# Performance work log

Measured on AMD Instinct MI355X. Metric: run time of the kernel, lower is better.

## Reference

```python
import jax, jax.numpy as jnp
import numpy as np

N, E, De, Dv = 40000, 8000, 32, 8   # nodes, hyperedges, edge degree, node degree
D, Q, EIG, VOC, NC = 256, 256, 64, 1000, 40  # vertex/edge dim, query dim, eig dim, centrality vocab, classes
LN_EPS = 1e-5


def _linear(x, W, b):
    return x @ W + b


def _layernorm(x, g, b):
    mu = jnp.mean(x, axis=-1, keepdims=True)
    var = jnp.mean(jnp.square(x - mu), axis=-1, keepdims=True)
    return (x - mu) * jax.lax.rsqrt(var + LN_EPS) * g + b


def setup_inputs() -> dict:
    key = jax.random.key(0)
    ks = iter(jax.random.split(key, 64))
    def nrm(shape, s=0.02):
        return (jax.random.normal(next(ks), shape, jnp.float32) * s).astype(jnp.float32)
    inp = {
        'vfeat': jax.random.normal(next(ks), (N, D), jnp.float32),
        'efeat': jax.random.normal(next(ks), (E, D), jnp.float32),
        'eign_vec': jax.random.normal(next(ks), (N, EIG), jnp.float32),
        'feat_v_gcn': jax.random.normal(next(ks), (N, D), jnp.float32),
        'cent1': jax.random.uniform(next(ks), (E, De), jnp.float32),
        'cent2': jax.random.uniform(next(ks), (N, Dv), jnp.float32),
        'cent_idx': jax.random.randint(next(ks), (N,), 0, VOC),
        'uniq_idx': jax.random.randint(next(ks), (N,), 0, VOC),
        'edge2node': jax.random.randint(next(ks), (E, De), 0, N),
        'node2edge': jax.random.randint(next(ks), (N, Dv), 0, E),
        # learned parameters (W: [in, out])
        'W_vtx': nrm((D, D)), 'b_vtx': jnp.zeros((D,), jnp.float32),
        'W_pe': nrm((EIG, D)), 'b_pe': jnp.zeros((D,), jnp.float32),
        'cs_emb': nrm((VOC, D)), 'un_emb': nrm((VOC, D)),
        'W_kv': nrm((D, Q)), 'b_kv': jnp.zeros((Q,), jnp.float32),
        'W_vv': nrm((D, D)), 'b_vv': jnp.zeros((D,), jnp.float32),
        'W_qe': nrm((D, Q)), 'b_qe': jnp.zeros((Q,), jnp.float32),
        'W_ke': nrm((D, Q)), 'b_ke': jnp.zeros((Q,), jnp.float32),
        'W_ve': nrm((D, D)), 'b_ve': jnp.zeros((D,), jnp.float32),
        'W_qv': nrm((D, Q)), 'b_qv': jnp.zeros((Q,), jnp.float32),
        'W_l1': nrm((D, Q)), 'b_l1': jnp.zeros((Q,), jnp.float32),
        'W_l2': nrm((Q, D)), 'b_l2': jnp.zeros((D,), jnp.float32),
        'W_l3': nrm((D, Q)), 'b_l3': jnp.zeros((Q,), jnp.float32),
        'W_l4': nrm((Q, D)), 'b_l4': jnp.zeros((D,), jnp.float32),
        'ln1_g': jnp.ones((D,), jnp.float32), 'ln1_b': jnp.zeros((D,), jnp.float32),
        'ln2_g': jnp.ones((D,), jnp.float32), 'ln2_b': jnp.zeros((D,), jnp.float32),
        'W_cls': nrm((D, NC)), 'b_cls': jnp.zeros((NC,), jnp.float32),
    }
    return inp


def _forward(vfeat, efeat, eign_vec, feat_v_gcn, cent1, cent2,
             W_vtx, b_vtx, W_pe, b_pe, cs_emb, un_emb,
             W_kv, b_kv, W_vv, b_vv, W_qe, b_qe, W_ke, b_ke, W_ve, b_ve, W_qv, b_qv,
             W_l1, b_l1, W_l2, b_l2, W_l3, b_l3, W_l4, b_l4,
             ln1_g, ln1_b, ln2_g, ln2_b, W_cls, b_cls,
             cent_idx, uniq_idx, edge2node, node2edge):
    scale = 1.0 / np.sqrt(float(W_kv.shape[1]))  # 1/sqrt(query_dim)
    # first_layer feature assembly: vtx_lin_1layer + PE + GCN + centrality/uniqueness embeddings
    feat_v = (_linear(vfeat, W_vtx, b_vtx) + _linear(eign_vec, W_pe, b_pe)
              + feat_v_gcn + cs_emb[cent_idx] + un_emb[uniq_idx])
    feat_e = efeat

    # ---- stage 1: hyperedges attend over member nodes ('in' etype) ----
    k_n = _linear(feat_v, W_kv, b_kv)              # [N,Q]
    v_n = _linear(feat_v, W_vv, b_vv)              # [N,D]
    q_e = _linear(feat_e, W_qe, b_qe)              # [E,Q]
    km = k_n[edge2node]                            # [E,De,Q]
    attn = jax.nn.leaky_relu(jnp.einsum('edq,eq->ed', km, q_e), 0.01) * scale
    score = jax.nn.softmax(attn + cent1, axis=1)   # centrality-biased softmax (k-core + clustering)
    h_e = jnp.einsum('ed,edc->ec', score, v_n[edge2node])  # [E,D]
    x_e = _layernorm(h_e + feat_e, ln1_g, ln1_b)
    f_e = _linear(jax.nn.relu(_linear(x_e, W_l1, b_l1)), W_l2, b_l2)
    feat_e = _layernorm(f_e + x_e, ln1_g, ln1_b)

    # ---- stage 2: nodes attend over incident hyperedges ('con' etype) ----
    k_e = _linear(feat_e, W_ke, b_ke)              # [E,Q]
    v_e = _linear(feat_e, W_ve, b_ve)              # [E,D]
    q_v = _linear(feat_v, W_qv, b_qv)              # [N,Q]
    km2 = k_e[node2edge]                           # [N,Dv,Q]
    attn2 = jax.nn.leaky_relu(jnp.einsum('ndq,nq->nd', km2, q_v), 0.01) * scale
    score2 = jax.nn.softmax(attn2 + cent2, axis=1)
    h_v = jnp.einsum('nd,ndc->nc', score2, v_e[node2edge])  # [N,D]
    x_v = _layernorm(h_v + feat_v, ln2_g, ln2_b)
    f_v = _linear(jax.nn.relu(_linear(x_v, W_l3, b_l3)), W_l4, b_l4)
    feat_v = _layernorm(f_v + x_v, ln2_g, ln2_b)

    # last_layer classification head (dropout is identity in eval)
    return _linear(feat_v, W_cls, b_cls)           # [N,NC]


def reference(vfeat, efeat, eign_vec, feat_v_gcn, cent1, cent2,
              cent_idx, uniq_idx, edge2node, node2edge,
              W_vtx, b_vtx, W_pe, b_pe, cs_emb, un_emb,
              W_kv, b_kv, W_vv, b_vv, W_qe, b_qe, W_ke, b_ke, W_ve, b_ve, W_qv, b_qv,
              W_l1, b_l1, W_l2, b_l2, W_l3, b_l3, W_l4, b_l4,
              ln1_g, ln1_b, ln2_g, ln2_b, W_cls, b_cls):
    return _forward(vfeat, efeat, eign_vec, feat_v_gcn, cent1, cent2,
                    W_vtx, b_vtx, W_pe, b_pe, cs_emb, un_emb,
                    W_kv, b_kv, W_vv, b_vv, W_qe, b_qe, W_ke, b_ke, W_ve, b_ve, W_qv, b_qv,
                    W_l1, b_l1, W_l2, b_l2, W_l3, b_l3, W_l4, b_l4,
                    ln1_g, ln1_b, ln2_g, ln2_b, W_cls, b_cls,
                    cent_idx, uniq_idx, edge2node, node2edge)
```

## Files before the change

kernel.cpp:

```cpp
#include <hip/hip_runtime.h>
#include <hip/hip_bf16.h>
#include <cstddef>

#define N_NODES 40000
#define N_EDGES 8000
#define DE 32
#define DV 8
#define DIM 256
#define QDIM 256
#define EIGD 64
#define NCLS 40
#define LN_EPS 1e-5f
#define ATT_SCALE 0.0625f

typedef unsigned short u16;
typedef unsigned int u32;
using i16x8 = __attribute__((ext_vector_type(8))) short;
using f32x4 = __attribute__((ext_vector_type(4))) float;

__device__ inline u16 f2b(float f) {
    union { float f; u32 u; } c; c.f = f;
    u32 u = c.u + 0x7FFF + ((c.u >> 16) & 1);
    return (u16)(u >> 16);
}
__device__ inline float b2f(u16 b) {
    union { u32 u; float f; } c; c.u = (u32)b << 16;
    return c.f;
}

__device__ inline void gload_lds16(const u16* g, u16* l) {
    __builtin_amdgcn_global_load_lds(
        (const __attribute__((address_space(1))) void*)g,
        (__attribute__((address_space(3))) void*)l, 16, 0, 0);
}

#define VMCNT12 asm volatile("s_waitcnt vmcnt(12)" ::: "memory")
#define VMCNT10 asm volatile("s_waitcnt vmcnt(10)" ::: "memory")
#define VMCNT6  asm volatile("s_waitcnt vmcnt(6)" ::: "memory")
#define VMCNT5  asm volatile("s_waitcnt vmcnt(5)" ::: "memory")
#define VMCNT4  asm volatile("s_waitcnt vmcnt(4)" ::: "memory")
#define VMCNT0  asm volatile("s_waitcnt vmcnt(0)" ::: "memory")
#define LGKM0   asm volatile("s_waitcnt lgkmcnt(0)" ::: "memory")

__global__ __launch_bounds__(256) void prep_weights(
    const float* w0, const float* w1, const float* w2, const float* w3,
    const float* w4, const float* w5, const float* w6, const float* w7,
    const float* w8, const float* w9, const float* w10, const float* w11,
    const float* w12, u16* __restrict__ pool)
{
    const float* srcs[13] = {w0,w1,w2,w3,w4,w5,w6,w7,w8,w9,w10,w11,w12};
    const int Ks[13]  = {256,64,256,256,256,256,256,256,256,256,256,256,256};
    const int Nds[13] = {256,256,256,256,256,256,256,256,256,256,256,256,40};
    const int id = blockIdx.z;
    const float* W = srcs[id];
    u16* Wt = pool + (size_t)id * 65536;
    const int K = Ks[id], Nd = Nds[id];
    const int k0 = blockIdx.x * 32, n0 = blockIdx.y * 32;
    if (k0 >= K || n0 >= Nd) return;

    __shared__ float tile[32][33];
    const int x = threadIdx.x & 31, y4 = (threadIdx.x >> 5) * 4;
#pragma unroll
    for (int j = 0; j < 4; j++) {
        int k = k0 + y4 + j;
        tile[y4 + j][x] = (k < K && (n0 + x) < Nd) ? W[(size_t)k * Nd + n0 + x] : 0.f;
    }
    __syncthreads();
#pragma unroll
    for (int j = 0; j < 4; j++) {
        int n = n0 + y4 + j;
        if (n < Nd && (k0 + x) < K)
            Wt[(size_t)n * K + k0 + x] = f2b(tile[x][y4 + j]);
    }
}

template <int EPI, int AMODE, int NT>
__global__ __launch_bounds__(256, 2) void gemmN(
    const void* __restrict__ Av, const u16* __restrict__ Wt,
    const float* __restrict__ bias0, const float* __restrict__ bias1,
    const float* __restrict__ bias2,
    void* __restrict__ Cv, int Nd)
{
    __shared__ u16 Asm[3][64 * 64];
    __shared__ u16 Bsm[3][128 * 64];
    const int t = threadIdx.x;
    const int lane = t & 63, w = t >> 6;
    const int wr = w >> 1, wc = w & 1;
    const int row0 = blockIdx.y * 64, col0 = blockIdx.x * 128;

    f32x4 acc[2][4] = {};

    const int srow = lane >> 3;
    const int sblk = ((lane & 7) ^ srow) * 8;
    const int fr = lane & 15, h = lane >> 4;
    const int lsw = fr & 7;

    float4 farA[2][2][2];

    auto stage_load = [&](int kt) {
        const int buf = kt % 3;
        const int k0 = kt << 6;
        if constexpr (AMODE == 0) {
#pragma unroll
            for (int i = 0; i < 2; i++) {
                const int r = w * 16 + i * 8;
                gload_lds16((const u16*)Av + (size_t)(row0 + r + srow) * 256 + k0 + sblk,
                            &Asm[buf][r * 64]);
            }
        } else {
#pragma unroll
            for (int i = 0; i < 2; i++) {
                const int r = w * 16 + i * 8;
                const float* ap = (const float*)Av + (size_t)(row0 + r + srow) * 256 + k0 + sblk;
                farA[kt & 1][i][0] = *(const float4*)ap;
                farA[kt & 1][i][1] = *(const float4*)(ap + 4);
            }
        }
#pragma unroll
        for (int i = 0; i < 4; i++) {
            const int r = w * 32 + i * 8;
            int ng = col0 + r + srow; if (ng > Nd - 1) ng = Nd - 1;
            gload_lds16(Wt + (size_t)ng * 256 + k0 + sblk, &Bsm[buf][r * 64]);
        }
    };
    auto stage_write = [&](int kt) {
        const int buf = kt % 3;
#pragma unroll
        for (int i = 0; i < 2; i++) {
            const int r = w * 16 + i * 8;
            float4 f0 = farA[kt & 1][i][0], f1 = farA[kt & 1][i][1];
            i16x8 v;
            v[0] = (short)f2b(f0.x); v[1] = (short)f2b(f0.y);
            v[2] = (short)f2b(f0.z); v[3] = (short)f2b(f0.w);
            v[4] = (short)f2b(f1.x); v[5] = (short)f2b(f1.y);
            v[6] = (short)f2b(f1.z); v[7] = (short)f2b(f1.w);
            *(i16x8*)&Asm[buf][(r + srow) * 64 + (lane & 7) * 8] = v;
        }
    };

    stage_load(0);
    if (NT > 1) stage_load(1);
    if constexpr (AMODE != 0) stage_write(0);

#pragma unroll
    for (int kt = 0; kt < NT; ++kt) {
        const int buf = kt % 3;
        if (kt + 2 < NT) stage_load(kt + 2);
        if constexpr (AMODE != 0) {
            if (kt + 1 < NT) stage_write(kt + 1);
            else { VMCNT0; }
        } else {
            if (kt + 2 < NT) { VMCNT12; }
            else if (kt + 1 < NT) { VMCNT6; }
            else { VMCNT0; }
        }
        __builtin_amdgcn_s_barrier();

        i16x8 af[2][2], bfr[2][4];
#pragma unroll
        for (int kk = 0; kk < 2; kk++) {
#pragma unroll
            for (int m = 0; m < 2; m++)
                af[kk][m] = *(const i16x8*)&Asm[buf][(wr * 32 + m * 16 + fr) * 64 +
                                                    ((kk * 4 + h) ^ lsw) * 8];
#pragma unroll
            for (int n = 0; n < 4; n++)
                bfr[kk][n] = *(const i16x8*)&Bsm[buf][(wc * 64 + n * 16 + fr) * 64 +
                                                     ((kk * 4 + h) ^ lsw) * 8];
        }
        LGKM0;
        __builtin_amdgcn_sched_barrier(0);
        __builtin_amdgcn_s_barrier();

#pragma unroll
        for (int kk = 0; kk < 2; kk++)
#pragma unroll
            for (int m = 0; m < 2; m++)
#pragma unroll
                for (int n = 0; n < 4; n++)
                    acc[m][n] = __builtin_amdgcn_mfma_f32_16x16x32_bf16(
                        af[kk][m], bfr[kk][n], acc[m][n], 0, 0, 0);
    }

    const int seg = (int)(blockIdx.x >> 1);
    const float* bp = (seg == 0) ? bias0 : ((seg == 1) ? bias1 : bias2);
#pragma unroll
    for (int m = 0; m < 2; m++) {
#pragma unroll
        for (int j = 0; j < 4; j++) {
            const int grow = row0 + wr * 32 + m * 16 + h * 4 + j;
#pragma unroll
            for (int n = 0; n < 4; n++) {
                const int gcol = col0 + wc * 64 + n * 16 + fr;
                if (EPI == 4 && gcol >= Nd) continue;
                float v = acc[m][n][j] + bp[gcol & 255];
                if constexpr (EPI == 1) v = fmaxf(v, 0.f);
                if constexpr (EPI == 4)
                    ((float*)Cv)[(size_t)grow * Nd + gcol] = v;
                else
                    ((u16*)Cv)[(size_t)grow * Nd + gcol] = f2b(v);
            }
        }
    }
}

template <int EPI, int AMODE, int NT>
__global__ __launch_bounds__(256, 2) void gemmW(
    const void* __restrict__ Av, const float* __restrict__ A2,
    const u16* __restrict__ Wt, const u16* __restrict__ Wt2,
    const float* __restrict__ bias0, const float* __restrict__ bias1,
    const u16* __restrict__ resid,
    const float* __restrict__ gcn, const float* __restrict__ emb1,
    const float* __restrict__ emb2, const int* __restrict__ idx1,
    const int* __restrict__ idx2, const float* __restrict__ lng,
    const float* __restrict__ lnb, u16* __restrict__ Cv)
{
    __shared__ u16 Asm[3][64 * 32];
    __shared__ u16 Bsm[3][256 * 32];
    const int t = threadIdx.x;
    const int lane = t & 63, w = t >> 6;
    const int row0 = blockIdx.y * 64;

    f32x4 acc[4][4] = {};

    const int srow = lane >> 2;
    const int sblk = ((lane & 3) ^ ((lane >> 3) & 3)) * 8;
    const int fr = lane & 15, h = lane >> 4;
    const int rsw = (fr >> 1) & 3;

    float4 farA[2][2];

    auto stage_load = [&](int kt) {
        const int buf = kt % 3;
        const int k0 = kt << 5;
        const bool tail = (AMODE == 2) && (k0 >= 256);
        if constexpr (AMODE == 0) {
            gload_lds16((const u16*)Av + (size_t)(row0 + w * 16 + srow) * 256 + k0 + sblk,
                        &Asm[buf][(w * 16) * 32]);
        } else {
            const float* ap = tail
                ? A2 + (size_t)(row0 + w * 16 + srow) * 64 + (k0 - 256) + sblk
                : (const float*)Av + (size_t)(row0 + w * 16 + srow) * 256 + k0 + sblk;
            farA[kt & 1][0] = *(const float4*)ap;
            farA[kt & 1][1] = *(const float4*)(ap + 4);
        }
#pragma unroll
        for (int i = 0; i < 4; i++) {
            const int r = w * 64 + i * 16;
            const u16* gp = tail ? Wt2 + (size_t)(r + srow) * 64 + (k0 - 256) + sblk
                                 : Wt + (size_t)(r + srow) * 256 + k0 + sblk;
            gload_lds16(gp, &Bsm[buf][r * 32]);
        }
    };
    auto stage_write = [&](int kt) {
        const int buf = kt % 3;
        float4 f0 = farA[kt & 1][0], f1 = farA[kt & 1][1];
        i16x8 v;
        v[0] = (short)f2b(f0.x); v[1] = (short)f2b(f0.y);
        v[2] = (short)f2b(f0.z); v[3] = (short)f2b(f0.w);
        v[4] = (short)f2b(f1.x); v[5] = (short)f2b(f1.y);
        v[6] = (short)f2b(f1.z); v[7] = (short)f2b(f1.w);
        *(i16x8*)&Asm[buf][(w * 16 + srow) * 32 + (lane & 3) * 8] = v;
    };

    stage_load(0);
    if (NT > 1) stage_load(1);
    if constexpr (AMODE != 0) stage_write(0);

#pragma unroll
    for (int kt = 0; kt < NT; ++kt) {
        const int buf = kt % 3;
        if (kt + 2 < NT) stage_load(kt + 2);
        if constexpr (AMODE != 0) {
            if (kt + 1 < NT) stage_write(kt + 1);
            else { VMCNT0; }
        } else {
            if (kt + 2 < NT) { VMCNT10; }
            else if (kt + 1 < NT) { VMCNT5; }
            else { VMCNT0; }
        }
        __builtin_amdgcn_s_barrier();

        i16x8 af[4], bfr[4];
#pragma unroll
        for (int m = 0; m < 4; m++)
            af[m] = *(const i16x8*)&Asm[buf][(m * 16 + fr) * 32 + (h ^ rsw) * 8];
#pragma unroll
        for (int n = 0; n < 4; n++)
            bfr[n] = *(const i16x8*)&Bsm[buf][(w * 64 + n * 16 + fr) * 32 + (h ^ rsw) * 8];
        LGKM0;
        __builtin_amdgcn_sched_barrier(0);
        __builtin_amdgcn_s_barrier();

#pragma unroll
        for (int m = 0; m < 4; m++)
#pragma unroll
            for (int n = 0; n < 4; n++)
                acc[m][n] = __builtin_amdgcn_mfma_f32_16x16x32_bf16(
                    af[m], bfr[n], acc[m][n], 0, 0, 0);
    }

    if constexpr (EPI == 5) {
        float* redS = (float*)&Asm[0][0];
        float* redQ = redS + 256;
#pragma unroll
        for (int m = 0; m < 4; m++) {
#pragma unroll
            for (int j = 0; j < 4; j++) {
                const int grow = row0 + m * 16 + h * 4 + j;
                float s = 0.f, q = 0.f;
#pragma unroll
                for (int n = 0; n < 4; n++) {
                    const int gcol = w * 64 + n * 16 + fr;
                    float v = acc[m][n][j] + bias0[gcol] +
                              b2f(resid[(size_t)grow * 256 + gcol]);
                    acc[m][n][j] = v;
                    s += v; q += v * v;
                }
#pragma unroll
                for (int off = 1; off < 16; off <<= 1) {
                    s += __shfl_xor(s, off, 64);
                    q += __shfl_xor(q, off, 64);
                }
                if (fr == 0) {
                    redS[(m * 16 + h * 4 + j) * 4 + w] = s;
                    redQ[(m * 16 + h * 4 + j) * 4 + w] = q;
                }
            }
        }
        __syncthreads();
#pragma unroll
        for (int m = 0; m < 4; m++) {
#pragma unroll
            for (int j = 0; j < 4; j++) {
                const int r = m * 16 + h * 4 + j;
                const int grow = row0 + r;
                float4 s4 = *(const float4*)&redS[r * 4];
                float4 q4 = *(const float4*)&redQ[r * 4];
                float mu = (s4.x + s4.y + s4.z + s4.w) * (1.f / DIM);
                float var = (q4.x + q4.y + q4.z + q4.w) * (1.f / DIM) - mu * mu;
                float rr = rsqrtf(var + LN_EPS);
#pragma unroll
                for (int n = 0; n < 4; n++) {
                    const int gcol = w * 64 + n * 16 + fr;
                    float y = (acc[m][n][j] - mu) * rr * lng[gcol] + lnb[gcol];
                    Cv[(size_t)grow * 256 + gcol] = f2b(y);
                }
            }
        }
    } else {
#pragma unroll
        for (int m = 0; m < 4; m++) {
#pragma unroll
            for (int j = 0; j < 4; j++) {
                const int grow = row0 + m * 16 + h * 4 + j;
                const int i1 = idx1[grow], i2 = idx2[grow];
#pragma unroll
                for (int n = 0; n < 4; n++) {
                    const int gcol = w * 64 + n * 16 + fr;
                    float v = acc[m][n][j] + bias0[gcol] + bias1[gcol];
                    v += gcn[(size_t)grow * 256 + gcol];
                    v += emb1[(size_t)i1 * 256 + gcol];
                    v += emb2[(size_t)i2 * 256 + gcol];
                    Cv[(size_t)grow * 256 + gcol] = f2b(v);
                }
            }
        }
    }
}

#define MST 264
template <int TAIL>
__global__ __launch_bounds__(256, 2) void ffn_fused(
    const u16* __restrict__ X, const u16* __restrict__ Wt1,
    const float* __restrict__ b1, const u16* __restrict__ Wt2,
    const float* __restrict__ b2, const float* __restrict__ lng,
    const float* __restrict__ lnb, const u16* __restrict__ WtT,
    const float* __restrict__ bT0, const float* __restrict__ bT1,
    void* __restrict__ outp)
{
    __shared__ __align__(16) u16 Asm[2][64 * 32];
    __shared__ __align__(16) u16 Bsm[2][256 * 32];
    __shared__ __align__(16) u16 Msm[64 * MST];
    const int t = threadIdx.x;
    const int lane = t & 63, w = t >> 6;
    const int row0 = blockIdx.x * 64;

    const int srow = lane >> 2;
    const int sblk = ((lane & 3) ^ ((lane >> 3) & 3)) * 8;
    const int fr = lane & 15, h = lane >> 4;
    const int rsw = (fr >> 1) & 3;

    f32x4 acc[4][4] = {};

    auto stageA = [&](int buf, int kt) {
        gload_lds16(X + (size_t)(row0 + w * 16 + srow) * 256 + (kt << 5) + sblk,
                    &Asm[buf][(w * 16) * 32]);
    };
    auto stageB = [&](int buf, int kt, const u16* W) {
#pragma unroll
        for (int i = 0; i < 4; i++) {
            const int r = w * 64 + i * 16;
            gload_lds16(W + (size_t)(r + srow) * 256 + (kt << 5) + sblk,
                        &Bsm[buf][r * 32]);
        }
    };

    stageA(0, 0); stageB(0, 0, Wt1);
#pragma unroll
    for (int kt = 0; kt < 8; ++kt) {
        const int buf = kt & 1;
        if (kt < 7) { stageA(buf ^ 1, kt + 1); stageB(buf ^ 1, kt + 1, Wt1); VMCNT5; }
        else { VMCNT0; }
        __builtin_amdgcn_s_barrier();

        i16x8 af[4], bfr[4];
#pragma unroll
        for (int m = 0; m < 4; m++)
            af[m] = *(const i16x8*)&Asm[buf][(m * 16 + fr) * 32 + (h ^ rsw) * 8];
#pragma unroll
        for (int n = 0; n < 4; n++)
            bfr[n] = *(const i16x8*)&Bsm[buf][(w * 64 + n * 16 + fr) * 32 + (h ^ rsw) * 8];
        LGKM0;
        __builtin_amdgcn_sched_barrier(0);
        __builtin_amdgcn_s_barrier();

#pragma unroll
        for (int m = 0; m < 4; m++)
#pragma unroll
            for (int n = 0; n < 4; n++)
                acc[m][n] = __builtin_amdgcn_mfma_f32_16x16x32_bf16(
                    af[m], bfr[n], acc[m][n], 0, 0, 0);
    }
    {
        float b1v[4];
#pragma unroll
        for (int n = 0; n < 4; n++) b1v[n] = b1[w * 64 + n * 16 + fr];
#pragma unroll
        for (int m = 0; m < 4; m++)
#pragma unroll
            for (int j = 0; j < 4; j++) {
                const int row = m * 16 + h * 4 + j;
#pragma unroll
                for (int n = 0; n < 4; n++) {
                    const int col = w * 64 + n * 16 + fr;
                    float v = fmaxf(acc[m][n][j] + b1v[n], 0.f);
                    Msm[row * MST + col] = f2b(v);
                    acc[m][n][j] = 0.f;
                }
            }
    }
    __syncthreads();

    stageB(0, 0, Wt2);
#pragma unroll
    for (int kt = 0; kt < 8; ++kt) {
        const int buf = kt & 1;
        if (kt < 7) { stageB(buf ^ 1, kt + 1, Wt2); VMCNT4; }
        else { VMCNT0; }
        __builtin_amdgcn_s_barrier();

        i16x8 af[4], bfr[4];
#pragma unroll
        for (int m = 0; m < 4; m++)
            af[m] = *(const i16x8*)&Msm[(m * 16 + fr) * MST + (kt << 5) + h * 8];
#pragma unroll
        for (int n = 0; n < 4; n++)
            bfr[n] = *(const i16x8*)&Bsm[buf][(w * 64 + n * 16 + fr) * 32 + (h ^ rsw) * 8];
        LGKM0;
        __builtin_amdgcn_sched_barrier(0);
        __builtin_amdgcn_s_barrier();

#pragma unroll
        for (int m = 0; m < 4; m++)
#pragma unroll
            for (int n = 0; n < 4; n++)
                acc[m][n] = __builtin_amdgcn_mfma_f32_16x16x32_bf16(
                    af[m], bfr[n], acc[m][n], 0, 0, 0);
    }
    {
        float* redS = (float*)&Asm[0][0];
        float* redQ = redS + 256;
#pragma unroll
        for (int m = 0; m < 4; m++) {
#pragma unroll
            for (int j = 0; j < 4; j++) {
                const int grow = row0 + m * 16 + h * 4 + j;
                float s = 0.f, q = 0.f;
#pragma unroll
                for (int n = 0; n < 4; n++) {
                    const int gcol = w * 64 + n * 16 + fr;
                    float v = acc[m][n][j] + b2[gcol] +
                              b2f(X[(size_t)grow * 256 + gcol]);
                    acc[m][n][j] = v;
                    s += v; q += v * v;
                }
#pragma unroll
                for (int off = 1; off < 16; off <<= 1) {
                    s += __shfl_xor(s, off, 64);
                    q += __shfl_xor(q, off, 64);
                }
                if (fr == 0) {
                    redS[(m * 16 + h * 4 + j) * 4 + w] = s;
                    redQ[(m * 16 + h * 4 + j) * 4 + w] = q;
                }
            }
        }
        __syncthreads();
#pragma unroll
        for (int m = 0; m < 4; m++) {
#pragma unroll
            for (int j = 0; j < 4; j++) {
                const int r = m * 16 + h * 4 + j;
                float4 s4 = *(const float4*)&redS[r * 4];
                float4 q4 = *(const float4*)&redQ[r * 4];
                float mu = (s4.x + s4.y + s4.z + s4.w) * (1.f / DIM);
                float var = (q4.x + q4.y + q4.z + q4.w) * (1.f / DIM) - mu * mu;
                float rr = rsqrtf(var + LN_EPS);
#pragma unroll
                for (int n = 0; n < 4; n++) {
                    const int gcol = w * 64 + n * 16 + fr;
                    float y = (acc[m][n][j] - mu) * rr * lng[gcol] + lnb[gcol];
                    acc[m][n][j] = y;
                }
            }
        }
        __syncthreads();
#pragma unroll
        for (int m = 0; m < 4; m++)
#pragma unroll
            for (int j = 0; j < 4; j++) {
                const int row = m * 16 + h * 4 + j;
#pragma unroll
                for (int n = 0; n < 4; n++)
                    Msm[row * MST + (w * 64 + n * 16 + fr)] = f2b(acc[m][n][j]);
            }
    }
    VMCNT0;
    __syncthreads();

    if constexpr (TAIL == 0) {
        u16* KVe = (u16*)outp;
#pragma unroll
        for (int half = 0; half < 2; half++) {
            const u16* Wb = WtT + (size_t)half * 256 * 256;
            const float* bT = half ? bT1 : bT0;
#pragma unroll
            for (int m = 0; m < 4; m++)
#pragma unroll
                for (int n = 0; n < 4; n++)
                    acc[m][n] = f32x4{0.f, 0.f, 0.f, 0.f};
            stageB(0, 0, Wb);
#pragma unroll
            for (int kt = 0; kt < 8; ++kt) {
                const int buf = kt & 1;
                if (kt < 7) { stageB(buf ^ 1, kt + 1, Wb); VMCNT4; }
                else { VMCNT0; }
                __builtin_amdgcn_s_barrier();

                i16x8 af[4], bfr[4];
#pragma unroll
                for (int m = 0; m < 4; m++)
                    af[m] = *(const i16x8*)&Msm[(m * 16 + fr) * MST + (kt << 5) + h * 8];
#pragma unroll
                for (int n = 0; n < 4; n++)
                    bfr[n] = *(const i16x8*)&Bsm[buf][(w * 64 + n * 16 + fr) * 32 + (h ^ rsw) * 8];
                LGKM0;
                __builtin_amdgcn_sched_barrier(0);
                __builtin_amdgcn_s_barrier();

#pragma unroll
                for (int m = 0; m < 4; m++)
#pragma unroll
                    for (int n = 0; n < 4; n++)
                        acc[m][n] = __builtin_amdgcn_mfma_f32_16x16x32_bf16(
                            af[m], bfr[n], acc[m][n], 0, 0, 0);
            }
#pragma unroll
            for (int m = 0; m < 4; m++)
#pragma unroll
                for (int j = 0; j < 4; j++) {
                    const int grow = row0 + m * 16 + h * 4 + j;
#pragma unroll
                    for (int n = 0; n < 4; n++) {
                        const int gcol = w * 64 + n * 16 + fr;
                        KVe[(size_t)grow * 512 + half * 256 + gcol] =
                            f2b(acc[m][n][j] + bT[gcol]);
                    }
                }
        }
    } else {
        float* out = (float*)outp;
        f32x4 acc3[3] = {};
#pragma unroll
        for (int kk = 0; kk < 8; kk++) {
            i16x8 af = *(const i16x8*)&Msm[(w * 16 + fr) * MST + kk * 32 + h * 8];
#pragma unroll
            for (int n = 0; n < 3; n++) {
                int br = n * 16 + fr; if (br > NCLS - 1) br = NCLS - 1;
                i16x8 bfr = *(const i16x8*)(WtT + (size_t)br * 256 + kk * 32 + h * 8);
                acc3[n] = __builtin_amdgcn_mfma_f32_16x16x32_bf16(af, bfr, acc3[n], 0, 0, 0);
            }
        }
#pragma unroll
        for (int n = 0; n < 3; n++) {
            const int gcol = n * 16 + fr;
            if (gcol >= NCLS) continue;
#pragma unroll
            for (int j = 0; j < 4; j++) {
                const int grow = row0 + w * 16 + h * 4 + j;
                out[(size_t)grow * NCLS + gcol] = acc3[n][j] + bT0[gcol];
            }
        }
    }
}

__global__ __launch_bounds__(256) void edge_attn(
    const u16* __restrict__ KVQn, const u16* __restrict__ QE,
    const float* __restrict__ efeat,
    const int* __restrict__ e2n, const float* __restrict__ cent1,
    const float* __restrict__ g, const float* __restrict__ bb,
    u16* __restrict__ XE)
{
    const int lane = threadIdx.x & 63, w = threadIdx.x >> 6;
    const int e = blockIdx.x * 4 + w;
    const int c4 = lane * 4;

    ushort4 q4 = *(const ushort4*)&QE[(size_t)e * QDIM + c4];
    const float q0 = b2f(q4.x), q1 = b2f(q4.y), q2 = b2f(q4.z), q3 = b2f(q4.w);

    int4 rv[8];
#pragma unroll
    for (int i = 0; i < 8; i++)
        rv[i] = *(const int4*)&e2n[(size_t)e * DE + i * 4];
    int rows[DE];
#pragma unroll
    for (int i = 0; i < 8; i++) {
        rows[i * 4 + 0] = rv[i].x; rows[i * 4 + 1] = rv[i].y;
        rows[i * 4 + 2] = rv[i].z; rows[i * 4 + 3] = rv[i].w;
    }

    float p[DE];
#pragma unroll
    for (int g0 = 0; g0 < DE; g0 += 16) {
        ushort4 k4[16];
#pragma unroll
        for (int j = 0; j < 16; j++)
            k4[j] = *(const ushort4*)&KVQn[(size_t)rows[g0 + j] * 768 + c4];
#pragma unroll
        for (int j = 0; j < 16; j++)
            p[g0 + j] = q0 * b2f(k4[j].x) + q1 * b2f(k4[j].y)
                      + q2 * b2f(k4[j].z) + q3 * b2f(k4[j].w);
    }
#pragma unroll
    for (int off = 32; off; off >>= 1)
#pragma unroll
        for (int d = 0; d < DE; d++)
            p[d] += __shfl_xor(p[d], off, 64);

    float4 cv[8];
#pragma unroll
    for (int i = 0; i < 8; i++)
        cv[i] = *(const float4*)&cent1[(size_t)e * DE + i * 4];
    float cent[DE];
#pragma unroll
    for (int i = 0; i < 8; i++) {
        cent[i * 4 + 0] = cv[i].x; cent[i * 4 + 1] = cv[i].y;
        cent[i * 4 + 2] = cv[i].z; cent[i * 4 + 3] = cv[i].w;
    }
#pragma unroll
    for (int d = 0; d < DE; d++)
        p[d] = (p[d] > 0.f ? p[d] : 0.01f * p[d]) * ATT_SCALE + cent[d];

    float mx = p[0];
#pragma unroll
    for (int d = 1; d < DE; d++) mx = fmaxf(mx, p[d]);
    float s = 0.f;
#pragma unroll
    for (int d = 0; d < DE; d++) { p[d] = __expf(p[d] - mx); s += p[d]; }
    const float inv = 1.f / s;
#pragma unroll
    for (int d = 0; d < DE; d++) p[d] *= inv;

    float a0 = 0.f, a1 = 0.f, a2 = 0.f, a3 = 0.f;
#pragma unroll
    for (int g0 = 0; g0 < DE; g0 += 16) {
        ushort4 v4[16];
#pragma unroll
        for (int j = 0; j < 16; j++)
            v4[j] = *(const ushort4*)&KVQn[(size_t)rows[g0 + j] * 768 + 256 + c4];
#pragma unroll
        for (int j = 0; j < 16; j++) {
            const float sd = p[g0 + j];
            a0 = fmaf(sd, b2f(v4[j].x), a0); a1 = fmaf(sd, b2f(v4[j].y), a1);
            a2 = fmaf(sd, b2f(v4[j].z), a2); a3 = fmaf(sd, b2f(v4[j].w), a3);
        }
    }
    float4 ef = *(const float4*)&efeat[(size_t)e * DIM + c4];
    float x0 = a0 + ef.x, x1 = a1 + ef.y, x2 = a2 + ef.z, x3 = a3 + ef.w;

    float mu = x0 + x1 + x2 + x3;
#pragma unroll
    for (int off = 32; off; off >>= 1) mu += __shfl_xor(mu, off, 64);
    mu *= (1.f / DIM);
    float d0 = x0 - mu, d1 = x1 - mu, d2 = x2 - mu, d3 = x3 - mu;
    float var = d0 * d0 + d1 * d1 + d2 * d2 + d3 * d3;
#pragma unroll
    for (int off = 32; off; off >>= 1) var += __shfl_xor(var, off, 64);
    var *= (1.f / DIM);
    float r = rsqrtf(var + LN_EPS);
    float4 gv = *(const float4*)&g[c4];
    float4 bv = *(const float4*)&bb[c4];
    ushort4 o;
    o.x = f2b(d0 * r * gv.x + bv.x); o.y = f2b(d1 * r * gv.y + bv.y);
    o.z = f2b(d2 * r * gv.z + bv.z); o.w = f2b(d3 * r * gv.w + bv.w);
    *(ushort4*)&XE[(size_t)e * DIM + c4] = o;
}

__global__ __launch_bounds__(256) void node_attn(
    const u16* __restrict__ KVe, const u16* __restrict__ KVQn,
    const u16* __restrict__ FV,
    const int* __restrict__ n2e, const float* __restrict__ cent2,
    const float* __restrict__ g, const float* __restrict__ bb,
    u16* __restrict__ XV)
{
    const int lane = threadIdx.x & 63, w = threadIdx.x >> 6;
    const int na = blockIdx.x * 8 + w * 2, nb = na + 1;
    const int c4 = lane * 4;

    ushort4 qa4 = *(const ushort4*)&KVQn[(size_t)na * 768 + 512 + c4];
    ushort4 qb4 = *(const ushort4*)&KVQn[(size_t)nb * 768 + 512 + c4];
    const float qa0 = b2f(qa4.x), qa1 = b2f(qa4.y), qa2 = b2f(qa4.z), qa3 = b2f(qa4.w);
    const float qb0 = b2f(qb4.x), qb1 = b2f(qb4.y), qb2 = b2f(qb4.z), qb3 = b2f(qb4.w);

    int4 r0 = *(const int4*)&n2e[(size_t)na * DV];
    int4 r1 = *(const int4*)&n2e[(size_t)na * DV + 4];
    int4 r2 = *(const int4*)&n2e[(size_t)nb * DV];
    int4 r3 = *(const int4*)&n2e[(size_t)nb * DV + 4];
    int rA[8] = {r0.x, r0.y, r0.z, r0.w, r1.x, r1.y, r1.z, r1.w};
    int rB[8] = {r2.x, r2.y, r2.z, r2.w, r3.x, r3.y, r3.z, r3.w};

    ushort4 kA[8], vA[8], kB[8], vB[8];
#pragma unroll
    for (int d = 0; d < DV; d++) {
        const u16* b = KVe + (size_t)rA[d] * 512 + c4;
        kA[d] = *(const ushort4*)b; vA[d] = *(const ushort4*)(b + 256);
    }
#pragma unroll
    for (int d = 0; d < DV; d++) {
        const u16* b = KVe + (size_t)rB[d] * 512 + c4;
        kB[d] = *(const ushort4*)b; vB[d] = *(const ushort4*)(b + 256);
    }

    float pA[8], pB[8];
#pragma unroll
    for (int d = 0; d < DV; d++) {
        pA[d] = qa0 * b2f(kA[d].x) + qa1 * b2f(kA[d].y)
              + qa2 * b2f(kA[d].z) + qa3 * b2f(kA[d].w);
        pB[d] = qb0 * b2f(kB[d].x) + qb1 * b2f(kB[d].y)
              + qb2 * b2f(kB[d].z) + qb3 * b2f(kB[d].w);
    }
#pragma unroll
    for (int off = 32; off; off >>= 1) {
#pragma unroll
        for (int d = 0; d < DV; d++) {
            pA[d] += __shfl_xor(pA[d], off, 64);
            pB[d] += __shfl_xor(pB[d], off, 64);
        }
    }
    float4 cA0 = *(const float4*)&cent2[(size_t)na * DV];
    float4 cA1 = *(const float4*)&cent2[(size_t)na * DV + 4];
    float4 cB0 = *(const float4*)&cent2[(size_t)nb * DV];
    float4 cB1 = *(const float4*)&cent2[(size_t)nb * DV + 4];
    float cA[8] = {cA0.x, cA0.y, cA0.z, cA0.w, cA1.x, cA1.y, cA1.z, cA1.w};
    float cB[8] = {cB0.x, cB0.y, cB0.z, cB0.w, cB1.x, cB1.y, cB1.z, cB1.w};
#pragma unroll
    for (int d = 0; d < DV; d++) {
        pA[d] = (pA[d] > 0.f ? pA[d] : 0.01f * pA[d]) * ATT_SCALE + cA[d];
        pB[d] = (pB[d] > 0.f ? pB[d] : 0.01f * pB[d]) * ATT_SCALE + cB[d];
    }
    float mA = pA[0], mB = pB[0];
#pragma unroll
    for (int d = 1; d < DV; d++) { mA = fmaxf(mA, pA[d]); mB = fmaxf(mB, pB[d]); }
    float sA = 0.f, sB = 0.f;
#pragma unroll
    for (int d = 0; d < DV; d++) {
        pA[d] = __expf(pA[d] - mA); sA += pA[d];
        pB[d] = __expf(pB[d] - mB); sB += pB[d];
    }
    const float iA = 1.f / sA, iB = 1.f / sB;

    float a0 = 0.f, a1 = 0.f, a2 = 0.f, a3 = 0.f;
    float b0 = 0.f, b1 = 0.f, b2 = 0.f, b3 = 0.f;
#pragma unroll
    for (int d = 0; d < DV; d++) {
        const float sa = pA[d] * iA, sb = pB[d] * iB;
        a0 = fmaf(sa, b2f(vA[d].x), a0); a1 = fmaf(sa, b2f(vA[d].y), a1);
        a2 = fmaf(sa, b2f(vA[d].z), a2); a3 = fmaf(sa, b2f(vA[d].w), a3);
        b0 = fmaf(sb, b2f(vB[d].x), b0); b1 = fmaf(sb, b2f(vB[d].y), b1);
        b2 = fmaf(sb, b2f(vB[d].z), b2); b3 = fmaf(sb, b2f(vB[d].w), b3);
    }
    ushort4 fa = *(const ushort4*)&FV[(size_t)na * DIM + c4];
    ushort4 fb = *(const ushort4*)&FV[(size_t)nb * DIM + c4];
    float xa0 = a0 + b2f(fa.x), xa1 = a1 + b2f(fa.y);
    float xa2 = a2 + b2f(fa.z), xa3 = a3 + b2f(fa.w);
    float xb0 = b0 + b2f(fb.x), xb1 = b1 + b2f(fb.y);
    float xb2 = b2 + b2f(fb.z), xb3 = b3 + b2f(fb.w);

    float muA = xa0 + xa1 + xa2 + xa3, muB = xb0 + xb1 + xb2 + xb3;
#pragma unroll
    for (int off = 32; off; off >>= 1) {
        muA += __shfl_xor(muA, off, 64);
        muB += __shfl_xor(muB, off, 64);
    }
    muA *= (1.f / DIM); muB *= (1.f / DIM);
    float da0 = xa0 - muA, da1 = xa1 - muA, da2 = xa2 - muA, da3 = xa3 - muA;
    float db0 = xb0 - muB, db1 = xb1 - muB, db2 = xb2 - muB, db3 = xb3 - muB;
    float vA_ = da0 * da0 + da1 * da1 + da2 * da2 + da3 * da3;
    float vB_ = db0 * db0 + db1 * db1 + db2 * db2 + db3 * db3;
#pragma unroll
    for (int off = 32; off; off >>= 1) {
        vA_ += __shfl_xor(vA_, off, 64);
        vB_ += __shfl_xor(vB_, off, 64);
    }
    const float rA_ = rsqrtf(vA_ * (1.f / DIM) + LN_EPS);
    const float rB_ = rsqrtf(vB_ * (1.f / DIM) + LN_EPS);
    float4 gv = *(const float4*)&g[c4];
    float4 bv = *(const float4*)&bb[c4];
    ushort4 oa, ob;
    oa.x = f2b(da0 * rA_ * gv.x + bv.x); oa.y = f2b(da1 * rA_ * gv.y + bv.y);
    oa.z = f2b(da2 * rA_ * gv.z + bv.z); oa.w = f2b(da3 * rA_ * gv.w + bv.w);
    ob.x = f2b(db0 * rB_ * gv.x + bv.x); ob.y = f2b(db1 * rB_ * gv.y + bv.y);
    ob.z = f2b(db2 * rB_ * gv.z + bv.z); ob.w = f2b(db3 * rB_ * gv.w + bv.w);
    *(ushort4*)&XV[(size_t)na * DIM + c4] = oa;
    *(ushort4*)&XV[(size_t)nb * DIM + c4] = ob;
}

extern "C" void kernel_launch(void* const* d_in, const int* in_sizes, int n_in,
                              void* d_out, int out_size, void* d_ws, size_t ws_size,
                              hipStream_t stream)
{
    const float* vfeat  = (const float*)d_in[0];
    const float* efeat  = (const float*)d_in[1];
    const float* eign   = (const float*)d_in[2];
    const float* gcn    = (const float*)d_in[3];
    const float* cent1  = (const float*)d_in[4];
    const float* cent2  = (const float*)d_in[5];
    const int*   cidx   = (const int*)d_in[6];
    const int*   uidx   = (const int*)d_in[7];
    const int*   e2n    = (const int*)d_in[8];
    const int*   n2e    = (const int*)d_in[9];
    const float* W_vtx  = (const float*)d_in[10]; const float* b_vtx = (const float*)d_in[11];
    const float* W_pe   = (const float*)d_in[12]; const float* b_pe  = (const float*)d_in[13];
    const float* cs_emb = (const float*)d_in[14]; const float* un_emb= (const float*)d_in[15];
    const float* W_kv   = (const float*)d_in[16]; const float* b_kv  = (const float*)d_in[17];
    const float* W_vv   = (const float*)d_in[18]; const float* b_vv  = (const float*)d_in[19];
    const float* W_qe   = (const float*)d_in[20]; const float* b_qe  = (const float*)d_in[21];
    const float* W_ke   = (const float*)d_in[22]; const float* b_ke  = (const float*)d_in[23];
    const float* W_ve   = (const float*)d_in[24]; const float* b_ve  = (const float*)d_in[25];
    const float* W_qv   = (const float*)d_in[26]; const float* b_qv  = (const float*)d_in[27];
    const float* W_l1   = (const float*)d_in[28]; const float* b_l1  = (const float*)d_in[29];
    const float* W_l2   = (const float*)d_in[30]; const float* b_l2  = (const float*)d_in[31];
    const float* W_l3   = (const float*)d_in[32]; const float* b_l3  = (const float*)d_in[33];
    const float* W_l4   = (const float*)d_in[34]; const float* b_l4  = (const float*)d_in[35];
    const float* ln1_g  = (const float*)d_in[36]; const float* ln1_b = (const float*)d_in[37];
    const float* ln2_g  = (const float*)d_in[38]; const float* ln2_b = (const float*)d_in[39];
    const float* W_cls  = (const float*)d_in[40]; const float* b_cls = (const float*)d_in[41];
    float* out = (float*)d_out;

    const size_t NE = (size_t)N_NODES * DIM;
    const size_t EE = (size_t)N_EDGES * DIM;
    u16* ws = (u16*)d_ws;
    u16* FVb  = ws;
    u16* KVQn = FVb + NE;
    u16* B2   = KVQn + 3 * NE;
    u16* QEb  = B2 + NE;
    u16* XE   = QEb + EE;
    u16* KVe  = XE + EE;
    u16* Wp   = KVe + 2 * EE;
    u16* Wt_vtx = Wp +  0 * 65536;
    u16* Wt_pe  = Wp +  1 * 65536;
    u16* Wt_kvq = Wp +  2 * 65536;
    u16* Wt_qe  = Wp +  5 * 65536;
    u16* Wt_kve = Wp +  6 * 65536;
    u16* Wt_l1  = Wp +  8 * 65536;
    u16* Wt_l2  = Wp +  9 * 65536;
    u16* Wt_l3  = Wp + 10 * 65536;
    u16* Wt_l4  = Wp + 11 * 65536;
    u16* Wt_cls = Wp + 12 * 65536;

    const dim3 blk(256);
    const dim3 gW(8, 8, 13);
    const dim3 gAsm(1, N_NODES / 64);
    const dim3 gKVQ(6, N_NODES / 64);
    const dim3 gQE(2, N_EDGES / 64);

    prep_weights<<<gW, blk, 0, stream>>>(
        W_vtx, W_pe, W_kv, W_vv, W_qv, W_qe, W_ke, W_ve,
        W_l1, W_l2, W_l3, W_l4, W_cls, Wp);

    gemmW<3, 2, 10><<<gAsm, blk, 0, stream>>>(vfeat, eign, Wt_vtx, Wt_pe,
        b_vtx, b_pe, nullptr, gcn, cs_emb, un_emb, cidx, uidx,
        nullptr, nullptr, FVb);

    gemmN<0, 0, 4><<<gKVQ, blk, 0, stream>>>(FVb, Wt_kvq,
        b_kv, b_vv, b_qv, KVQn, 768);
    gemmN<0, 1, 4><<<gQE, blk, 0, stream>>>(efeat, Wt_qe,
        b_qe, b_qe, b_qe, QEb, 256);
    edge_attn<<<N_EDGES / 4, blk, 0, stream>>>(KVQn, QEb, efeat, e2n, cent1,
        ln1_g, ln1_b, XE);
    ffn_fused<0><<<N_EDGES / 64, blk, 0, stream>>>(XE, Wt_l1, b_l1,
        Wt_l2, b_l2, ln1_g, ln1_b, Wt_kve, b_ke, b_ve, KVe);

    node_attn<<<N_NODES / 8, blk, 0, stream>>>(KVe, KVQn, FVb, n2e, cent2,
        ln2_g, ln2_b, B2);
    ffn_fused<1><<<N_NODES / 64, blk, 0, stream>>>(B2, Wt_l3, b_l3,
        Wt_l4, b_l4, ln2_g, ln2_b, Wt_cls, b_cls, nullptr, out);
}
```

Baseline: 239.3 us.

## Fuse vertex assembly GEMM with KVQ projection in one kernel

Replaces the separate assembly GEMM (vfeat/eigvec projection plus gcn and embedding adds) and the following KVQ GEMM with one kernel. The assembled 64-row bf16 tile stays in LDS and feeds three 256-column projections directly, so FVb is not re-read from global memory and one launch is removed. The embedding and gcn adds are now done with vectorized float4 loads instead of scattered per-element reads. In exchange, each block runs the three KVQ chunks serially over fewer blocks, uses a double-buffered pipeline instead of triple buffering, and carries the extra Msm LDS footprint, which may lower occupancy. An extra LGKM wait is also added in gemmN.

New measurement: 237.3 us. No clear change (-0.8%).

```diff
diff --git a/kernel.cpp b/kernel.cpp
--- a/kernel.cpp
+++ b/kernel.cpp
@@ -35,7 +35,6 @@
 }
 
 #define VMCNT12 asm volatile("s_waitcnt vmcnt(12)" ::: "memory")
-#define VMCNT10 asm volatile("s_waitcnt vmcnt(10)" ::: "memory")
 #define VMCNT6  asm volatile("s_waitcnt vmcnt(6)" ::: "memory")
 #define VMCNT5  asm volatile("s_waitcnt vmcnt(5)" ::: "memory")
 #define VMCNT4  asm volatile("s_waitcnt vmcnt(4)" ::: "memory")
@@ -74,6 +73,192 @@
     }
 }
 
+#define MST 264
+__global__ __launch_bounds__(256, 2) void asm_kvq(
+    const float* __restrict__ vfeat, const float* __restrict__ eign,
+    const u16* __restrict__ Wt_vtx, const u16* __restrict__ Wt_pe,
+    const float* __restrict__ b_vtx, const float* __restrict__ b_pe,
+    const float* __restrict__ gcn, const float* __restrict__ emb1,
+    const float* __restrict__ emb2, const int* __restrict__ idx1,
+    const int* __restrict__ idx2,
+    const u16* __restrict__ Wt_kvq, const float* __restrict__ b_kv,
+    const float* __restrict__ b_vv, const float* __restrict__ b_qv,
+    u16* __restrict__ FVb, u16* __restrict__ KVQn)
+{
+    __shared__ __align__(16) u16 Asm[2][64 * 32];
+    __shared__ __align__(16) u16 Bsm[2][256 * 32];
+    __shared__ __align__(16) u16 Msm[64 * MST];
+    const int t = threadIdx.x;
+    const int lane = t & 63, w = t >> 6;
+    const int row0 = blockIdx.x * 64;
+
+    const int srow = lane >> 2;
+    const int sblk = ((lane & 3) ^ ((lane >> 3) & 3)) * 8;
+    const int fr = lane & 15, h = lane >> 4;
+    const int rsw = (fr >> 1) & 3;
+
+    f32x4 acc[4][4] = {};
+    float4 fA[2][2];
+
+    auto p1_issueB = [&](int kt) {
+        const int buf = kt & 1;
+        const int k0 = kt << 5;
+        const bool tail = (k0 >= 256);
+#pragma unroll
+        for (int i = 0; i < 4; i++) {
+            const int r = w * 64 + i * 16;
+            const u16* gp = tail ? Wt_pe + (size_t)(r + srow) * 64 + (k0 - 256) + sblk
+                                 : Wt_vtx + (size_t)(r + srow) * 256 + k0 + sblk;
+            gload_lds16(gp, &Bsm[buf][r * 32]);
+        }
+    };
+    auto p1_loadA = [&](int kt) {
+        const int k0 = kt << 5;
+        const bool tail = (k0 >= 256);
+        const float* ap = tail
+            ? eign + (size_t)(row0 + w * 16 + srow) * 64 + (k0 - 256) + sblk
+            : vfeat + (size_t)(row0 + w * 16 + srow) * 256 + k0 + sblk;
+        fA[kt & 1][0] = *(const float4*)ap;
+        fA[kt & 1][1] = *(const float4*)(ap + 4);
+    };
+    auto p1_write = [&](int kt) {
+        const int buf = kt & 1;
+        float4 f0 = fA[buf][0], f1 = fA[buf][1];
+        i16x8 v;
+        v[0] = (short)f2b(f0.x); v[1] = (short)f2b(f0.y);
+        v[2] = (short)f2b(f0.z); v[3] = (short)f2b(f0.w);
+        v[4] = (short)f2b(f1.x); v[5] = (short)f2b(f1.y);
+        v[6] = (short)f2b(f1.z); v[7] = (short)f2b(f1.w);
+        *(i16x8*)&Asm[buf][(w * 16 + srow) * 32 + (lane & 3) * 8] = v;
+    };
+
+    p1_loadA(0); p1_issueB(0); p1_loadA(1); p1_write(0);
+#pragma unroll
+    for (int kt = 0; kt < 10; ++kt) {
+        const int buf = kt & 1;
+        if (kt + 1 < 10) p1_issueB(kt + 1);
+        if (kt + 2 < 10) p1_loadA(kt + 2);
+        if (kt + 1 < 10) p1_write(kt + 1);
+        else { VMCNT0; }
+        LGKM0;
+        __builtin_amdgcn_s_barrier();
+
+        i16x8 af[4], bfr[4];
+#pragma unroll
+        for (int m = 0; m < 4; m++)
+            af[m] = *(const i16x8*)&Asm[buf][(m * 16 + fr) * 32 + (h ^ rsw) * 8];
+#pragma unroll
+        for (int n = 0; n < 4; n++)
+            bfr[n] = *(const i16x8*)&Bsm[buf][(w * 64 + n * 16 + fr) * 32 + (h ^ rsw) * 8];
+        LGKM0;
+        __builtin_amdgcn_sched_barrier(0);
+        __builtin_amdgcn_s_barrier();
+
+#pragma unroll
+        for (int m = 0; m < 4; m++)
+#pragma unroll
+            for (int n = 0; n < 4; n++)
+                acc[m][n] = __builtin_amdgcn_mfma_f32_16x16x32_bf16(
+                    af[m], bfr[n], acc[m][n], 0, 0, 0);
+    }
+
+#pragma unroll
+    for (int m = 0; m < 4; m++)
+#pragma unroll
+        for (int j = 0; j < 4; j++) {
+            const int row = m * 16 + h * 4 + j;
+#pragma unroll
+            for (int n = 0; n < 4; n++) {
+                const int col = w * 64 + n * 16 + fr;
+                float v = acc[m][n][j] + b_vtx[col] + b_pe[col];
+                Msm[row * MST + col] = f2b(v);
+                acc[m][n][j] = 0.f;
+            }
+        }
+    __syncthreads();
+
+    const float4* gcn4 = (const float4*)gcn;
+    const float4* e1_4 = (const float4*)emb1;
+    const float4* e2_4 = (const float4*)emb2;
+    ushort4* FVb4 = (ushort4*)FVb;
+#pragma unroll 4
+    for (int it = 0; it < 16; ++it) {
+        const int T = t + it * 256;
+        const int row = T >> 6, cg = T & 63;
+        const int grow = row0 + row;
+        const int i1 = idx1[grow], i2 = idx2[grow];
+        ushort4 mv = *(const ushort4*)&Msm[row * MST + cg * 4];
+        float4 gv = gcn4[(size_t)grow * 64 + cg];
+        float4 e1 = e1_4[(size_t)i1 * 64 + cg];
+        float4 e2 = e2_4[(size_t)i2 * 64 + cg];
+        ushort4 o;
+        o.x = f2b(b2f(mv.x) + gv.x + e1.x + e2.x);
+        o.y = f2b(b2f(mv.y) + gv.y + e1.y + e2.y);
+        o.z = f2b(b2f(mv.z) + gv.z + e1.z + e2.z);
+        o.w = f2b(b2f(mv.w) + gv.w + e1.w + e2.w);
+        FVb4[(size_t)grow * 64 + cg] = o;
+        *(ushort4*)&Msm[row * MST + cg * 4] = o;
+    }
+    __syncthreads();
+
+    auto p2_issueB = [&](int buf, int kt, const u16* Wb) {
+#pragma unroll
+        for (int i = 0; i < 4; i++) {
+            const int r = w * 64 + i * 16;
+            gload_lds16(Wb + (size_t)(r + srow) * 256 + (kt << 5) + sblk,
+                        &Bsm[buf][r * 32]);
+        }
+    };
+#pragma unroll 1
+    for (int c = 0; c < 3; ++c) {
+        const u16* Wb = Wt_kvq + (size_t)c * 256 * 256;
+        const float* bc = (c == 0) ? b_kv : ((c == 1) ? b_vv : b_qv);
+#pragma unroll
+        for (int m = 0; m < 4; m++)
+#pragma unroll
+            for (int n = 0; n < 4; n++)
+                acc[m][n] = f32x4{0.f, 0.f, 0.f, 0.f};
+        p2_issueB(0, 0, Wb);
+#pragma unroll
+        for (int kt = 0; kt < 8; ++kt) {
+            const int buf = kt & 1;
+            if (kt < 7) { p2_issueB(buf ^ 1, kt + 1, Wb); VMCNT4; }
+            else { VMCNT0; }
+            __builtin_amdgcn_s_barrier();
+
+            i16x8 af[4], bfr[4];
+#pragma unroll
+            for (int m = 0; m < 4; m++)
+                af[m] = *(const i16x8*)&Msm[(m * 16 + fr) * MST + (kt << 5) + h * 8];
+#pragma unroll
+            for (int n = 0; n < 4; n++)
+                bfr[n] = *(const i16x8*)&Bsm[buf][(w * 64 + n * 16 + fr) * 32 + (h ^ rsw) * 8];
+            LGKM0;
+            __builtin_amdgcn_sched_barrier(0);
+            __builtin_amdgcn_s_barrier();
+
+#pragma unroll
+            for (int m = 0; m < 4; m++)
+#pragma unroll
+                for (int n = 0; n < 4; n++)
+                    acc[m][n] = __builtin_amdgcn_mfma_f32_16x16x32_bf16(
+                        af[m], bfr[n], acc[m][n], 0, 0, 0);
+        }
+#pragma unroll
+        for (int m = 0; m < 4; m++)
+#pragma unroll
+            for (int j = 0; j < 4; j++) {
+                const int grow = row0 + m * 16 + h * 4 + j;
+#pragma unroll
+                for (int n = 0; n < 4; n++) {
+                    const int gcol = w * 64 + n * 16 + fr;
+                    KVQn[(size_t)grow * 768 + c * 256 + gcol] =
+                        f2b(acc[m][n][j] + bc[gcol]);
+                }
+            }
+    }
+}
+
 template <int EPI, int AMODE, int NT>
 __global__ __launch_bounds__(256, 2) void gemmN(
     const void* __restrict__ Av, const u16* __restrict__ Wt,
@@ -154,6 +339,7 @@
             else if (kt + 1 < NT) { VMCNT6; }
             else { VMCNT0; }
         }
+        LGKM0;
         __builtin_amdgcn_s_barrier();
 
         i16x8 af[2][2], bfr[2][4];
@@ -204,172 +390,6 @@
     }
 }
 
-template <int EPI, int AMODE, int NT>
-__global__ __launch_bounds__(256, 2) void gemmW(
-    const void* __restrict__ Av, const float* __restrict__ A2,
-    const u16* __restrict__ Wt, const u16* __restrict__ Wt2,
-    const float* __restrict__ bias0, const float* __restrict__ bias1,
-    const u16* __restrict__ resid,
-    const float* __restrict__ gcn, const float* __restrict__ emb1,
-    const float* __restrict__ emb2, const int* __restrict__ idx1,
-    const int* __restrict__ idx2, const float* __restrict__ lng,
-    const float* __restrict__ lnb, u16* __restrict__ Cv)
-{
-    __shared__ u16 Asm[3][64 * 32];
-    __shared__ u16 Bsm[3][256 * 32];
-    const int t = threadIdx.x;
-    const int lane = t & 63, w = t >> 6;
-    const int row0 = blockIdx.y * 64;
-
-    f32x4 acc[4][4] = {};
-
-    const int srow = lane >> 2;
-    const int sblk = ((lane & 3) ^ ((lane >> 3) & 3)) * 8;
-    const int fr = lane & 15, h = lane >> 4;
-    const int rsw = (fr >> 1) & 3;
-
-    float4 farA[2][2];
-
-    auto stage_load = [&](int kt) {
-        const int buf = kt % 3;
-        const int k0 = kt << 5;
-        const bool tail = (AMODE == 2) && (k0 >= 256);
-        if constexpr (AMODE == 0) {
-            gload_lds16((const u16*)Av + (size_t)(row0 + w * 16 + srow) * 256 + k0 + sblk,
-                        &Asm[buf][(w * 16) * 32]);
-        } else {
-            const float* ap = tail
-                ? A2 + (size_t)(row0 + w * 16 + srow) * 64 + (k0 - 256) + sblk
-                : (const float*)Av + (size_t)(row0 + w * 16 + srow) * 256 + k0 + sblk;
-            farA[kt & 1][0] = *(const float4*)ap;
-            farA[kt & 1][1] = *(const float4*)(ap + 4);
-        }
-#pragma unroll
-        for (int i = 0; i < 4; i++) {
-            const int r = w * 64 + i * 16;
-            const u16* gp = tail ? Wt2 + (size_t)(r + srow) * 64 + (k0 - 256) + sblk
-                                 : Wt + (size_t)(r + srow) * 256 + k0 + sblk;
-            gload_lds16(gp, &Bsm[buf][r * 32]);
-        }
-    };
-    auto stage_write = [&](int kt) {
-        const int buf = kt % 3;
-        float4 f0 = farA[kt & 1][0], f1 = farA[kt & 1][1];
-        i16x8 v;
-        v[0] = (short)f2b(f0.x); v[1] = (short)f2b(f0.y);
-        v[2] = (short)f2b(f0.z); v[3] = (short)f2b(f0.w);
-        v[4] = (short)f2b(f1.x); v[5] = (short)f2b(f1.y);
-        v[6] = (short)f2b(f1.z); v[7] = (short)f2b(f1.w);
-        *(i16x8*)&Asm[buf][(w * 16 + srow) * 32 + (lane & 3) * 8] = v;
-    };
-
-    stage_load(0);
-    if (NT > 1) stage_load(1);
-    if constexpr (AMODE != 0) stage_write(0);
-
-#pragma unroll
-    for (int kt = 0; kt < NT; ++kt) {
-        const int buf = kt % 3;
-        if (kt + 2 < NT) stage_load(kt + 2);
-        if constexpr (AMODE != 0) {
-            if (kt + 1 < NT) stage_write(kt + 1);
-            else { VMCNT0; }
-        } else {
-            if (kt + 2 < NT) { VMCNT10; }
-            else if (kt + 1 < NT) { VMCNT5; }
-            else { VMCNT0; }
-        }
-        __builtin_amdgcn_s_barrier();
-
-        i16x8 af[4], bfr[4];
-#pragma unroll
-        for (int m = 0; m < 4; m++)
-            af[m] = *(const i16x8*)&Asm[buf][(m * 16 + fr) * 32 + (h ^ rsw) * 8];
-#pragma unroll
-        for (int n = 0; n < 4; n++)
-            bfr[n] = *(const i16x8*)&Bsm[buf][(w * 64 + n * 16 + fr) * 32 + (h ^ rsw) * 8];
-        LGKM0;
-        __builtin_amdgcn_sched_barrier(0);
-        __builtin_amdgcn_s_barrier();
-
-#pragma unroll
-        for (int m = 0; m < 4; m++)
-#pragma unroll
-            for (int n = 0; n < 4; n++)
-                acc[m][n] = __builtin_amdgcn_mfma_f32_16x16x32_bf16(
-                    af[m], bfr[n], acc[m][n], 0, 0, 0);
-    }
-
-    if constexpr (EPI == 5) {
-        float* redS = (float*)&Asm[0][0];
-        float* redQ = redS + 256;
-#pragma unroll
-        for (int m = 0; m < 4; m++) {
-#pragma unroll
-            for (int j = 0; j < 4; j++) {
-                const int grow = row0 + m * 16 + h * 4 + j;
-                float s = 0.f, q = 0.f;
-#pragma unroll
-                for (int n = 0; n < 4; n++) {
-                    const int gcol = w * 64 + n * 16 + fr;
-                    float v = acc[m][n][j] + bias0[gcol] +
-                              b2f(resid[(size_t)grow * 256 + gcol]);
-                    acc[m][n][j] = v;
-                    s += v; q += v * v;
-                }
-#pragma unroll
-                for (int off = 1; off < 16; off <<= 1) {
-                    s += __shfl_xor(s, off, 64);
-                    q += __shfl_xor(q, off, 64);
-                }
-                if (fr == 0) {
-                    redS[(m * 16 + h * 4 + j) * 4 + w] = s;
-                    redQ[(m * 16 + h * 4 + j) * 4 + w] = q;
-                }
-            }
-        }
-        __syncthreads();
-#pragma unroll
-        for (int m = 0; m < 4; m++) {
-#pragma unroll
-            for (int j = 0; j < 4; j++) {
-                const int r = m * 16 + h * 4 + j;
-                const int grow = row0 + r;
-                float4 s4 = *(const float4*)&redS[r * 4];
-                float4 q4 = *(const float4*)&redQ[r * 4];
-                float mu = (s4.x + s4.y + s4.z + s4.w) * (1.f / DIM);
-                float var = (q4.x + q4.y + q4.z + q4.w) * (1.f / DIM) - mu * mu;
-                float rr = rsqrtf(var + LN_EPS);
-#pragma unroll
-                for (int n = 0; n < 4; n++) {
-                    const int gcol = w * 64 + n * 16 + fr;
-                    float y = (acc[m][n][j] - mu) * rr * lng[gcol] + lnb[gcol];
-                    Cv[(size_t)grow * 256 + gcol] = f2b(y);
-                }
-            }
-        }
-    } else {
-#pragma unroll
-        for (int m = 0; m < 4; m++) {
-#pragma unroll
-            for (int j = 0; j < 4; j++) {
-                const int grow = row0 + m * 16 + h * 4 + j;
-                const int i1 = idx1[grow], i2 = idx2[grow];
-#pragma unroll
-                for (int n = 0; n < 4; n++) {
-                    const int gcol = w * 64 + n * 16 + fr;
-                    float v = acc[m][n][j] + bias0[gcol] + bias1[gcol];
-                    v += gcn[(size_t)grow * 256 + gcol];
-                    v += emb1[(size_t)i1 * 256 + gcol];
-                    v += emb2[(size_t)i2 * 256 + gcol];
-                    Cv[(size_t)grow * 256 + gcol] = f2b(v);
-                }
-            }
-        }
-    }
-}
-
-#define MST 264
 template <int TAIL>
 __global__ __launch_bounds__(256, 2) void ffn_fused(
     const u16* __restrict__ X, const u16* __restrict__ Wt1,
@@ -891,20 +911,17 @@
 
     const dim3 blk(256);
     const dim3 gW(8, 8, 13);
-    const dim3 gAsm(1, N_NODES / 64);
-    const dim3 gKVQ(6, N_NODES / 64);
     const dim3 gQE(2, N_EDGES / 64);
 
     prep_weights<<<gW, blk, 0, stream>>>(
         W_vtx, W_pe, W_kv, W_vv, W_qv, W_qe, W_ke, W_ve,
         W_l1, W_l2, W_l3, W_l4, W_cls, Wp);
 
-    gemmW<3, 2, 10><<<gAsm, blk, 0, stream>>>(vfeat, eign, Wt_vtx, Wt_pe,
-        b_vtx, b_pe, nullptr, gcn, cs_emb, un_emb, cidx, uidx,
-        nullptr, nullptr, FVb);
-
-    gemmN<0, 0, 4><<<gKVQ, blk, 0, stream>>>(FVb, Wt_kvq,
-        b_kv, b_vv, b_qv, KVQn, 768);
+    asm_kvq<<<N_NODES / 64, blk, 0, stream>>>(
+        vfeat, eign, Wt_vtx, Wt_pe, b_vtx, b_pe,
+        gcn, cs_emb, un_emb, cidx, uidx,
+        Wt_kvq, b_kv, b_vv, b_qv, FVb, KVQn);
+
     gemmN<0, 1, 4><<<gQE, blk, 0, stream>>>(efeat, Wt_qe,
         b_qe, b_qe, b_qe, QEb, 256);
     edge_attn<<<N_EDGES / 4, blk, 0, stream>>>(KVQn, QEb, efeat, e2n, cent1,
```
